# Performance work log

Measured on AMD Instinct MI355X. Metric: run time of the kernel, lower is better.

## Reference

```python
import jax, jax.numpy as jnp
import numpy as np
from jax import lax

B, C, H, W = 8, 256, 128, 128


def _scan_along(x, decay, axis):
    """Linear decay recurrence s_t = decay*s_{t-1} + (1-decay)*x_t along `axis`.

    x: [B, C, H, W]; decay: [C] (constant per channel).
    """
    xm = jnp.moveaxis(x, axis, 0)          # [L, B, C, rest]
    d = decay.reshape(1, -1, 1)            # broadcast over [B, C, rest]
    one_minus_d = 1.0 - d

    def step(state, cur):
        state = d * state + one_minus_d * cur
        return state, state

    init = jnp.zeros_like(xm[0])
    _, ys = lax.scan(step, init, xm)
    return jnp.moveaxis(ys, 0, axis)


def setup_inputs() -> dict:
    key = jax.random.key(0)
    k1, k2, k3, k4 = jax.random.split(key, 4)
    x = jax.random.normal(k1, (B, C, H, W), dtype=jnp.float32)
    decay_logits = 0.5 * jax.random.normal(k2, (4, C), dtype=jnp.float32)
    mix_logits = 0.5 * jax.random.normal(k3, (4, C), dtype=jnp.float32)
    input_scale = 0.5 * jax.random.normal(k4, (4, C), dtype=jnp.float32)
    return {"x": x, "decay_logits": decay_logits,
            "mix_logits": mix_logits, "input_scale": input_scale}


def reference(x, decay_logits, mix_logits, input_scale):
    decay = jnp.clip(jax.nn.sigmoid(decay_logits), 0.05, 0.995)   # [4, C]
    mix = jax.nn.softmax(mix_logits, axis=0)                       # [4, C]
    scale = 1.0 + jnp.tanh(input_scale)                            # [4, C]

    def sc(d):  # per-channel [C] -> broadcastable [1, C, 1, 1]
        return d.reshape(1, -1, 1, 1)

    # left -> right: scan along width (axis 3)
    lr = _scan_along(x * sc(scale[0]), decay[0], axis=3)
    # right -> left: flip width, scan, flip back
    rl = jnp.flip(_scan_along(jnp.flip(x, axis=3) * sc(scale[1]), decay[1], axis=3), axis=3)
    # top -> bottom: scan along height (axis 2)
    tb = _scan_along(x * sc(scale[2]), decay[2], axis=2)
    # bottom -> top: flip height, scan, flip back
    bt = jnp.flip(_scan_along(jnp.flip(x, axis=2) * sc(scale[3]), decay[3], axis=2), axis=2)

    return sc(mix[0]) * lr + sc(mix[1]) * rl + sc(mix[2]) * tb + sc(mix[3]) * bt
```

## Files before the change

kernel.cpp:

```cpp
#include <hip/hip_runtime.h>

#define CH 256
#define HH 128
#define WW 128
#define HW (HH * WW)
#define SEGH 16
#define NSEG 8

__global__ __launch_bounds__(1024, 4) void dscan_kernel(
    const float* __restrict__ x,
    const float* __restrict__ decay_logits,
    const float* __restrict__ mix_logits,
    const float* __restrict__ input_scale,
    float* __restrict__ out)
{
    extern __shared__ float smem[];
    float* __restrict__ xs  = smem;
    float* __restrict__ scr = smem + HW;

    const int img  = blockIdx.x;
    const int c    = img & (CH - 1);
    const int tid  = threadIdx.x;
    const int lane = tid & 63;
    const int wv   = tid >> 6;

    const float dl0 = decay_logits[0 * CH + c];
    const float dl1 = decay_logits[1 * CH + c];
    const float dl2 = decay_logits[2 * CH + c];
    const float dl3 = decay_logits[3 * CH + c];
    const float ml0 = mix_logits[0 * CH + c];
    const float ml1 = mix_logits[1 * CH + c];
    const float ml2 = mix_logits[2 * CH + c];
    const float ml3 = mix_logits[3 * CH + c];
    const float il0 = input_scale[0 * CH + c];
    const float il1 = input_scale[1 * CH + c];
    const float il2 = input_scale[2 * CH + c];
    const float il3 = input_scale[3 * CH + c];

    const float d0 = fminf(fmaxf(1.0f / (1.0f + expf(-dl0)), 0.05f), 0.995f);
    const float d1 = fminf(fmaxf(1.0f / (1.0f + expf(-dl1)), 0.05f), 0.995f);
    const float d2 = fminf(fmaxf(1.0f / (1.0f + expf(-dl2)), 0.05f), 0.995f);
    const float d3 = fminf(fmaxf(1.0f / (1.0f + expf(-dl3)), 0.05f), 0.995f);

    const float mmax = fmaxf(fmaxf(ml0, ml1), fmaxf(ml2, ml3));
    const float e0 = expf(ml0 - mmax);
    const float e1 = expf(ml1 - mmax);
    const float e2 = expf(ml2 - mmax);
    const float e3 = expf(ml3 - mmax);
    const float einv = 1.0f / (e0 + e1 + e2 + e3);
    const float m0 = e0 * einv, m1 = e1 * einv, m2 = e2 * einv, m3 = e3 * einv;

    const float sc0 = 1.0f + tanhf(il0);
    const float sc1 = 1.0f + tanhf(il1);
    const float sc2 = 1.0f + tanhf(il2);
    const float sc3 = 1.0f + tanhf(il3);

    const float c0 = (1.0f - d0) * sc0;
    const float c1 = (1.0f - d1) * sc1;
    const float c2 = (1.0f - d2) * sc2;
    const float c3 = (1.0f - d3) * sc3;

    const float d0p4 = (d0 * d0) * (d0 * d0);
    const float d1p4 = (d1 * d1) * (d1 * d1);
    float q0[5], q1[5];
    q0[0] = d0p4; q1[0] = d1p4;
#pragma unroll
    for (int k = 1; k < 5; ++k) { q0[k] = q0[k-1] * q0[k-1]; q1[k] = q1[k-1] * q1[k-1]; }

    float t2 = d2 * d2; t2 = t2 * t2; t2 = t2 * t2; const float d2p16 = t2 * t2;
    float t3 = d3 * d3; t3 = t3 * t3; t3 = t3 * t3; const float d3p16 = t3 * t3;

    const float* __restrict__ xg = x + (size_t)img * HW;
    float* __restrict__ og = out + (size_t)img * HW;

    {
        const int sl   = lane & 31;
        const int half = lane >> 5;
        const int rbase = (wv << 1) + half;

        float4 v[4];
#pragma unroll
        for (int it = 0; it < 4; ++it)
            v[it] = *(const float4*)(xg + ((it << 5) + rbase) * WW + (sl << 2));

#pragma unroll
        for (int it = 0; it < 4; ++it) {
            const int r = (it << 5) + rbase;
            const float4 xv4 = v[it];

            float bL = c0 * xv4.x;
            bL = fmaf(d0, bL, c0 * xv4.y);
            bL = fmaf(d0, bL, c0 * xv4.z);
            bL = fmaf(d0, bL, c0 * xv4.w);
            float bR = c1 * xv4.w;
            bR = fmaf(d1, bR, c1 * xv4.z);
            bR = fmaf(d1, bR, c1 * xv4.y);
            bR = fmaf(d1, bR, c1 * xv4.x);

#pragma unroll
            for (int k = 0; k < 5; ++k) {
                const int off = 1 << k;
                const float bU = __shfl_up(bL, (unsigned)off, 32);
                bL = fmaf(q0[k], (sl >= off) ? bU : 0.0f, bL);
                const float bD = __shfl_down(bR, (unsigned)off, 32);
                bR = fmaf(q1[k], (sl < 32 - off) ? bD : 0.0f, bR);
            }
            float EL = __shfl_up(bL, 1u, 32);
            if (sl == 0) EL = 0.0f;
            float ER = __shfl_down(bR, 1u, 32);
            if (sl == 31) ER = 0.0f;

            const float l0 = fmaf(d0, EL, c0 * xv4.x);
            const float l1 = fmaf(d0, l0, c0 * xv4.y);
            const float l2 = fmaf(d0, l1, c0 * xv4.z);
            const float l3 = fmaf(d0, l2, c0 * xv4.w);
            const float r3 = fmaf(d1, ER, c1 * xv4.w);
            const float r2 = fmaf(d1, r3, c1 * xv4.z);
            const float r1 = fmaf(d1, r2, c1 * xv4.y);
            const float r0 = fmaf(d1, r1, c1 * xv4.x);

            float4 o4;
            o4.x = fmaf(m0, l0, m1 * r0);
            o4.y = fmaf(m0, l1, m1 * r1);
            o4.z = fmaf(m0, l2, m1 * r2);
            o4.w = fmaf(m0, l3, m1 * r3);
            *(float4*)(xs + r * WW + (sl << 2)) = o4;
        }
    }

    const int col = tid & (WW - 1);
    const int seg = tid >> 7;
    const float* __restrict__ xcol = xg + seg * SEGH * WW + col;
    {
        float b2 = 0.0f, b3 = 0.0f, pw = c3;
#pragma unroll
        for (int i = 0; i < SEGH; ++i) {
            const float xv = xcol[i * WW];
            b2 = fmaf(d2, b2, c2 * xv);
            b3 = fmaf(pw, xv, b3);
            pw *= d3;
        }
        scr[tid]        = b2;
        scr[1024 + tid] = b3;
    }

    __syncthreads();

    float Sin = 0.0f;
    for (int j = 0; j < seg; ++j)
        Sin = fmaf(d2p16, Sin, scr[j * WW + col]);
    float Tin = 0.0f;
    for (int j = NSEG - 1; j > seg; --j)
        Tin = fmaf(d3p16, Tin, scr[1024 + j * WW + col]);

    {
        float xv[SEGH], tb[SEGH];
        float s = Sin;
#pragma unroll
        for (int i = 0; i < SEGH; ++i) {
            const float v = xcol[i * WW];
            xv[i] = v;
            s = fmaf(d2, s, c2 * v);
            tb[i] = s;
        }
        float t = Tin;
        float* __restrict__ ocol = og + seg * SEGH * WW + col;
        const float* __restrict__ pcol = xs + seg * SEGH * WW + col;
#pragma unroll
        for (int i = SEGH - 1; i >= 0; --i) {
            t = fmaf(d3, t, c3 * xv[i]);
            const float hres = pcol[i * WW];
            ocol[i * WW] = fmaf(m2, tb[i], fmaf(m3, t, hres));
        }
    }
}

extern "C" void kernel_launch(void* const* d_in, const int* in_sizes, int n_in,
                              void* d_out, int out_size, void* d_ws, size_t ws_size,
                              hipStream_t stream) {
    const float* x  = (const float*)d_in[0];
    const float* dl = (const float*)d_in[1];
    const float* ml = (const float*)d_in[2];
    const float* is = (const float*)d_in[3];
    float* out = (float*)d_out;

    const size_t lds_bytes = (size_t)(HW + 2048) * sizeof(float);

    static bool attr_set = false;
    if (!attr_set) {
        (void)hipFuncSetAttribute((const void*)dscan_kernel,
                                  hipFuncAttributeMaxDynamicSharedMemorySize,
                                  (int)lds_bytes);
        attr_set = true;
    }

    dim3 grid(2048), block(1024);
    hipLaunchKernelGGL(dscan_kernel, grid, block, lds_bytes, stream, x, dl, ml, is, out);
}
```

Baseline: 245.7 us.

## Compute per-channel params across lanes, keep column x in registers, relax launch bounds

Measured after the change: 239.3 us. 1.03x faster.

```diff
diff --git a/kernel.cpp b/kernel.cpp
--- a/kernel.cpp
+++ b/kernel.cpp
@@ -7,7 +7,14 @@
 #define SEGH 16
 #define NSEG 8
 
-__global__ __launch_bounds__(1024, 4) void dscan_kernel(
+__device__ __forceinline__ float rdlane(float v, int l) {
+    return __int_as_float(__builtin_amdgcn_readlane(__float_as_int(v), l));
+}
+__device__ __forceinline__ float uni(float v) {
+    return __int_as_float(__builtin_amdgcn_readfirstlane(__float_as_int(v)));
+}
+
+__global__ __launch_bounds__(1024, 2) void dscan_kernel(
     const float* __restrict__ x,
     const float* __restrict__ decay_logits,
     const float* __restrict__ mix_logits,
@@ -24,51 +31,50 @@
     const int lane = tid & 63;
     const int wv   = tid >> 6;
 
-    const float dl0 = decay_logits[0 * CH + c];
-    const float dl1 = decay_logits[1 * CH + c];
-    const float dl2 = decay_logits[2 * CH + c];
-    const float dl3 = decay_logits[3 * CH + c];
-    const float ml0 = mix_logits[0 * CH + c];
-    const float ml1 = mix_logits[1 * CH + c];
-    const float ml2 = mix_logits[2 * CH + c];
-    const float ml3 = mix_logits[3 * CH + c];
-    const float il0 = input_scale[0 * CH + c];
-    const float il1 = input_scale[1 * CH + c];
-    const float il2 = input_scale[2 * CH + c];
-    const float il3 = input_scale[3 * CH + c];
-
-    const float d0 = fminf(fmaxf(1.0f / (1.0f + expf(-dl0)), 0.05f), 0.995f);
-    const float d1 = fminf(fmaxf(1.0f / (1.0f + expf(-dl1)), 0.05f), 0.995f);
-    const float d2 = fminf(fmaxf(1.0f / (1.0f + expf(-dl2)), 0.05f), 0.995f);
-    const float d3 = fminf(fmaxf(1.0f / (1.0f + expf(-dl3)), 0.05f), 0.995f);
-
-    const float mmax = fmaxf(fmaxf(ml0, ml1), fmaxf(ml2, ml3));
-    const float e0 = expf(ml0 - mmax);
-    const float e1 = expf(ml1 - mmax);
-    const float e2 = expf(ml2 - mmax);
-    const float e3 = expf(ml3 - mmax);
-    const float einv = 1.0f / (e0 + e1 + e2 + e3);
-    const float m0 = e0 * einv, m1 = e1 * einv, m2 = e2 * einv, m3 = e3 * einv;
-
-    const float sc0 = 1.0f + tanhf(il0);
-    const float sc1 = 1.0f + tanhf(il1);
-    const float sc2 = 1.0f + tanhf(il2);
-    const float sc3 = 1.0f + tanhf(il3);
-
-    const float c0 = (1.0f - d0) * sc0;
-    const float c1 = (1.0f - d1) * sc1;
-    const float c2 = (1.0f - d2) * sc2;
-    const float c3 = (1.0f - d3) * sc3;
-
-    const float d0p4 = (d0 * d0) * (d0 * d0);
-    const float d1p4 = (d1 * d1) * (d1 * d1);
+    float pv = 0.0f;
+    {
+        const int j = lane & 3;
+        const int g = lane >> 2;
+        if (g == 0) {
+            const float v = decay_logits[j * CH + c];
+            pv = fminf(fmaxf(1.0f / (1.0f + expf(-v)), 0.05f), 0.995f);
+        } else if (g == 1) {
+            const float a0 = mix_logits[0 * CH + c];
+            const float a1 = mix_logits[1 * CH + c];
+            const float a2 = mix_logits[2 * CH + c];
+            const float a3 = mix_logits[3 * CH + c];
+            const float mm = fmaxf(fmaxf(a0, a1), fmaxf(a2, a3));
+            const float aj = (j == 0) ? a0 : (j == 1) ? a1 : (j == 2) ? a2 : a3;
+            pv = expf(aj - mm);
+        } else if (g == 2) {
+            pv = 1.0f + tanhf(input_scale[j * CH + c]);
+        }
+    }
+    const float d0 = rdlane(pv, 0), d1 = rdlane(pv, 1);
+    const float d2 = rdlane(pv, 2), d3 = rdlane(pv, 3);
+    const float e0 = rdlane(pv, 4), e1 = rdlane(pv, 5);
+    const float e2 = rdlane(pv, 6), e3 = rdlane(pv, 7);
+    const float s0 = rdlane(pv, 8), s1 = rdlane(pv, 9);
+    const float s2 = rdlane(pv, 10), s3 = rdlane(pv, 11);
+
+    const float einv = uni(1.0f / (e0 + e1 + e2 + e3));
+    const float m0 = uni(e0 * einv), m1 = uni(e1 * einv);
+    const float m2 = uni(e2 * einv), m3 = uni(e3 * einv);
+    const float c0 = uni((1.0f - d0) * s0);
+    const float c1 = uni((1.0f - d1) * s1);
+    const float c2 = uni((1.0f - d2) * s2);
+    const float c3 = uni((1.0f - d3) * s3);
+
     float q0[5], q1[5];
-    q0[0] = d0p4; q1[0] = d1p4;
-#pragma unroll
-    for (int k = 1; k < 5; ++k) { q0[k] = q0[k-1] * q0[k-1]; q1[k] = q1[k-1] * q1[k-1]; }
-
-    float t2 = d2 * d2; t2 = t2 * t2; t2 = t2 * t2; const float d2p16 = t2 * t2;
-    float t3 = d3 * d3; t3 = t3 * t3; t3 = t3 * t3; const float d3p16 = t3 * t3;
+    q0[0] = uni((d0 * d0) * (d0 * d0));
+    q1[0] = uni((d1 * d1) * (d1 * d1));
+#pragma unroll
+    for (int k = 1; k < 5; ++k) {
+        q0[k] = uni(q0[k-1] * q0[k-1]);
+        q1[k] = uni(q1[k-1] * q1[k-1]);
+    }
+    float t2v = d2 * d2; t2v = t2v * t2v; t2v = t2v * t2v; const float d2p16 = uni(t2v * t2v);
+    float t3v = d3 * d3; t3v = t3v * t3v; t3v = t3v * t3v; const float d3p16 = uni(t3v * t3v);
 
     const float* __restrict__ xg = x + (size_t)img * HW;
     float* __restrict__ og = out + (size_t)img * HW;
@@ -131,15 +137,21 @@
     const int col = tid & (WW - 1);
     const int seg = tid >> 7;
     const float* __restrict__ xcol = xg + seg * SEGH * WW + col;
-    {
-        float b2 = 0.0f, b3 = 0.0f, pw = c3;
-#pragma unroll
-        for (int i = 0; i < SEGH; ++i) {
-            const float xv = xcol[i * WW];
-            b2 = fmaf(d2, b2, c2 * xv);
-            b3 = fmaf(pw, xv, b3);
-            pw *= d3;
-        }
+
+    float xv[SEGH];
+    {
+#pragma unroll
+        for (int i = 0; i < SEGH; ++i) xv[i] = xcol[i * WW];
+
+        float b2 = 0.0f;
+#pragma unroll
+        for (int i = 0; i < SEGH; ++i) b2 = fmaf(d2, b2, c2 * xv[i]);
+
+        float b3 = 0.0f;
+#pragma unroll
+        for (int i = SEGH - 1; i >= 0; --i) b3 = fmaf(d3, b3, xv[i]);
+        b3 *= c3;
+
         scr[tid]        = b2;
         scr[1024 + tid] = b3;
     }
@@ -154,23 +166,20 @@
         Tin = fmaf(d3p16, Tin, scr[1024 + j * WW + col]);
 
     {
-        float xv[SEGH], tb[SEGH];
+        float* __restrict__ pcol = xs + seg * SEGH * WW + col;
+        float* __restrict__ ocol = og + seg * SEGH * WW + col;
+
         float s = Sin;
 #pragma unroll
         for (int i = 0; i < SEGH; ++i) {
-            const float v = xcol[i * WW];
-            xv[i] = v;
-            s = fmaf(d2, s, c2 * v);
-            tb[i] = s;
+            s = fmaf(d2, s, c2 * xv[i]);
+            pcol[i * WW] = fmaf(m2, s, pcol[i * WW]);
         }
         float t = Tin;
-        float* __restrict__ ocol = og + seg * SEGH * WW + col;
-        const float* __restrict__ pcol = xs + seg * SEGH * WW + col;
 #pragma unroll
         for (int i = SEGH - 1; i >= 0; --i) {
             t = fmaf(d3, t, c3 * xv[i]);
-            const float hres = pcol[i * WW];
-            ocol[i * WW] = fmaf(m2, tb[i], fmaf(m3, t, hres));
+            ocol[i * WW] = fmaf(m3, t, pcol[i * WW]);
         }
     }
 }
```
